# Performance work log

Hardware: AMD Instinct MI355X
Metric: run time of the kernel (lower is better)

## Reference

```python
import jax, jax.numpy as jnp
import numpy as np

N_NODES = 100_000
N_EDGES = 1_600_000
N_GRAPHS = 512
D_NODE = 128
H = 128
L_EXTRA = 2  # model_layer - 1


def _bn(x, g, b, eps=1e-5):
    # BatchNorm1d, training-mode math (biased batch variance), eval dropout = identity
    mu = jnp.mean(x, axis=0)
    var = jnp.var(x, axis=0)
    return g * (x - mu) * jax.lax.rsqrt(var + eps) + b


def _gin_conv(x, src, dst, W1, b1, bng, bnb, W2, b2):
    # GINConv (eps=0): mlp(x + sum_{j->i} x_j); mlp = Lin -> BN -> ReLU -> Lin
    agg = jax.ops.segment_sum(x[src], dst, num_segments=x.shape[0])
    h = x + agg
    h = jax.nn.relu(_bn(h @ W1 + b1, bng, bnb))
    return h @ W2 + b2


def setup_inputs():
    key = jax.random.key(0)
    ks = jax.random.split(key, 24)
    s = 0.05
    d = {}
    d["x"] = jax.random.normal(ks[0], (N_NODES, D_NODE), dtype=jnp.float32)
    d["edge_index"] = jax.random.randint(ks[1], (2, N_EDGES), 0, N_NODES, dtype=jnp.int32)
    d["batch"] = jnp.sort(jax.random.randint(ks[2], (N_NODES,), 0, N_GRAPHS, dtype=jnp.int32))
    d["vn_emb"] = jax.random.normal(ks[3], (1, H)) * s
    # conv1 MLP: Linear(D_NODE, 2H) -> BN -> ReLU -> Linear(2H, H)
    d["c1_W1"] = jax.random.normal(ks[4], (D_NODE, 2 * H)) * s
    d["c1_b1"] = jnp.zeros((2 * H,))
    d["c1_bng"] = jnp.ones((2 * H,))
    d["c1_bnb"] = jnp.zeros((2 * H,))
    d["c1_W2"] = jax.random.normal(ks[5], (2 * H, H)) * s
    d["c1_b2"] = jnp.zeros((H,))
    d["bn1_g"] = jnp.ones((H,))
    d["bn1_b"] = jnp.zeros((H,))
    # stacked extra GIN layers (model_layer - 1)
    d["cW1"] = jax.random.normal(ks[6], (L_EXTRA, H, 2 * H)) * s
    d["cb1"] = jnp.zeros((L_EXTRA, 2 * H))
    d["cbng"] = jnp.ones((L_EXTRA, 2 * H))
    d["cbnb"] = jnp.zeros((L_EXTRA, 2 * H))
    d["cW2"] = jax.random.normal(ks[7], (L_EXTRA, 2 * H, H)) * s
    d["cb2"] = jnp.zeros((L_EXTRA, H))
    d["bns_g"] = jnp.ones((L_EXTRA, H))
    d["bns_b"] = jnp.zeros((L_EXTRA, H))
    # virtual node MLP: Lin(H,2H)->BN->ReLU->Lin(2H,H)->BN->ReLU->Dropout
    d["vW1"] = jax.random.normal(ks[8], (H, 2 * H)) * s
    d["vb1"] = jnp.zeros((2 * H,))
    d["vbn1_g"] = jnp.ones((2 * H,))
    d["vbn1_b"] = jnp.zeros((2 * H,))
    d["vW2"] = jax.random.normal(ks[9], (2 * H, H)) * s
    d["vb2"] = jnp.zeros((H,))
    d["vbn2_g"] = jnp.ones((H,))
    d["vbn2_b"] = jnp.zeros((H,))
    return d


def reference(x, edge_index, batch, vn_emb, c1_W1, c1_b1, c1_bng, c1_bnb, c1_W2, c1_b2,
              bn1_g, bn1_b, cW1, cb1, cbng, cbnb, cW2, cb2, bns_g, bns_b,
              vW1, vb1, vbn1_g, vbn1_b, vW2, vb2, vbn2_g, vbn2_b):
    src, dst = edge_index[0], edge_index[1]
    # virtual node feature per graph: Embedding(1, H) indexed with zeros
    vfeat = jnp.broadcast_to(vn_emb[0], (N_GRAPHS, H))
    # layer 1: dropout is identity in eval mode
    post = jax.nn.relu(_bn(_gin_conv(x, src, dst, c1_W1, c1_b1, c1_bng, c1_bnb, c1_W2, c1_b2), bn1_g, bn1_b))
    for i in range(L_EXTRA):
        post = post + vfeat[batch]                       # virtual-node broadcast
        post = _bn(_gin_conv(post, src, dst, cW1[i], cb1[i], cbng[i], cbnb[i], cW2[i], cb2[i]), bns_g[i], bns_b[i])
        if i < L_EXTRA - 1:
            post = jax.nn.relu(post)
            pooled = jax.ops.segment_sum(post, batch, num_segments=N_GRAPHS)  # GlobalAddPool
            z = pooled + vfeat
            z = jax.nn.relu(_bn(z @ vW1 + vb1, vbn1_g, vbn1_b))
            vfeat = jax.nn.relu(_bn(z @ vW2 + vb2, vbn2_g, vbn2_b))
    # readout: global mean pool over nodes per graph
    counts = jax.ops.segment_sum(jnp.ones((x.shape[0],), post.dtype), batch, num_segments=N_GRAPHS)
    out = jax.ops.segment_sum(post, batch, num_segments=N_GRAPHS) / jnp.maximum(counts, 1.0)[:, None]
    return out
```

## Files before the change

### kernel.cpp

```cpp
#include <hip/hip_runtime.h>

#define NN 100000
#define NE 1600000
#define NG 512
#define DH 128
#define DH2 256
#define SCB 98
#define NSTRIPE 32

typedef __attribute__((ext_vector_type(8))) _Float16 h8;
typedef __attribute__((ext_vector_type(2))) _Float16 h2;
typedef __attribute__((ext_vector_type(4))) float f4;

static inline size_t align256(size_t x) { return (x + 255) & ~size_t(255); }

__global__ __launch_bounds__(256) void countslot_k(const int* __restrict__ ei,
                                                   int* __restrict__ cursor,
                                                   int* __restrict__ slot) {
    int i = blockIdx.x * blockDim.x + threadIdx.x;
    int stride = gridDim.x * blockDim.x;
    for (int e = i; e < NE; e += stride)
        slot[e] = atomicAdd(&cursor[ei[NE + e]], 1);
}

__global__ __launch_bounds__(256) void place_k(const int* __restrict__ ei,
                                               const int* __restrict__ rowptr,
                                               const int* __restrict__ slot,
                                               int* __restrict__ esrc) {
    int i = blockIdx.x * blockDim.x + threadIdx.x;
    int stride = gridDim.x * blockDim.x;
    for (int e = i; e < NE; e += stride)
        esrc[rowptr[ei[NE + e]] + slot[e]] = ei[e];
}

__global__ void gbound_k(const int* __restrict__ batch, int* __restrict__ gcnt) {
    int g = blockIdx.x * blockDim.x + threadIdx.x;
    if (g >= NG) return;
    int lo = 0, hi = NN;
    while (lo < hi) { int m = (lo + hi) >> 1; if (batch[m] < g) lo = m + 1; else hi = m; }
    int b0 = lo;
    lo = 0; hi = NN;
    int g1 = g + 1;
    while (lo < hi) { int m = (lo + hi) >> 1; if (batch[m] < g1) lo = m + 1; else hi = m; }
    gcnt[g] = lo - b0;
}

__global__ __launch_bounds__(256) void scan1_k(const int* __restrict__ deg,
                                               int* __restrict__ part) {
    int i0 = blockIdx.x * 1024 + threadIdx.x * 4;
    int s = 0;
    if (i0 < NN) {
        int4 v = *(const int4*)(deg + i0);
        s = v.x + v.y + v.z + v.w;
    }
#pragma unroll
    for (int o = 1; o < 64; o <<= 1) s += __shfl_xor(s, o);
    __shared__ int ws[4];
    if ((threadIdx.x & 63) == 0) ws[threadIdx.x >> 6] = s;
    __syncthreads();
    if (threadIdx.x == 0) part[blockIdx.x] = ws[0] + ws[1] + ws[2] + ws[3];
}

__global__ void scan2_k(int* __restrict__ part, int* __restrict__ rowptr) {
    int t = threadIdx.x;
    int v = (t < SCB) ? part[t] : 0;
    int s = v;
#pragma unroll
    for (int o = 1; o < 64; o <<= 1) {
        int u = __shfl_up(s, o);
        if ((t & 63) >= o) s += u;
    }
    __shared__ int wtot[2];
    if ((t & 63) == 63) wtot[t >> 6] = s;
    __syncthreads();
    if (t >= 64) s += wtot[0];
    if (t < SCB) part[t] = s - v;
    if (t == SCB - 1) rowptr[NN] = s;
}

__global__ __launch_bounds__(256) void scan3_k(const int* __restrict__ deg,
                                               const int* __restrict__ part,
                                               int* __restrict__ rowptr) {
    int t = threadIdx.x;
    int i0 = blockIdx.x * 1024 + t * 4;
    int4 v = {0, 0, 0, 0};
    if (i0 < NN) v = *(const int4*)(deg + i0);
    int s = v.x + v.y + v.z + v.w;
    __shared__ int sc[256];
    sc[t] = s;
    __syncthreads();
    for (int o = 1; o < 256; o <<= 1) {
        int add = (t >= o) ? sc[t - o] : 0;
        __syncthreads();
        sc[t] += add;
        __syncthreads();
    }
    int excl = (t ? sc[t - 1] : 0) + part[blockIdx.x];
    if (i0 < NN) {
        int4 r;
        r.x = excl;
        r.y = excl + v.x;
        r.z = excl + v.x + v.y;
        r.w = excl + v.x + v.y + v.z;
        *(int4*)(rowptr + i0) = r;
    }
}

__global__ void castx_k(const float* __restrict__ x, _Float16* __restrict__ xh) {
    int i = blockIdx.x * blockDim.x + threadIdx.x;
    if (i >= NN * 16) return;
    const float4* s = (const float4*)x + i * 2;
    float4 p = s[0], q = s[1];
    h8 h = {(_Float16)p.x, (_Float16)p.y, (_Float16)p.z, (_Float16)p.w,
            (_Float16)q.x, (_Float16)q.y, (_Float16)q.z, (_Float16)q.w};
    ((h8*)xh)[i] = h;
}

__global__ void vinit_k(const float* __restrict__ emb, _Float16* __restrict__ vfeat) {
    int i = blockIdx.x * blockDim.x + threadIdx.x;
    if (i < NG * DH) vfeat[i] = (_Float16)emb[i & (DH - 1)];
}

__global__ void zin_k(const float* __restrict__ pooled, const _Float16* __restrict__ vf,
                      _Float16* __restrict__ zb) {
    int i = blockIdx.x * blockDim.x + threadIdx.x;
    if (i < NG * DH) zb[i] = (_Float16)(pooled[i] + (float)vf[i]);
}

__global__ void addvn_k(_Float16* __restrict__ x, const _Float16* __restrict__ vfeat,
                        const int* __restrict__ batch) {
    int i = blockIdx.x * blockDim.x + threadIdx.x;
    if (i >= NN * 16) return;
    int row = i >> 4;
    int bg = batch[row];
    h8 u = ((h8*)x)[i];
    h8 v = ((const h8*)vfeat)[bg * 16 + (i & 15)];
    h8 o;
#pragma unroll
    for (int e = 0; e < 8; e++) o[e] = (_Float16)((float)u[e] + (float)v[e]);
    ((h8*)x)[i] = o;
}

__global__ void finalout_k(const float* __restrict__ pooled2, const int* __restrict__ gcnt,
                           float* __restrict__ outp) {
    int i = blockIdx.x * blockDim.x + threadIdx.x;
    if (i >= NG * DH) return;
    float cnt = (float)gcnt[i >> 7];
    outp[i] = pooled2[i] / fmaxf(cnt, 1.0f);
}

struct WPack {
    const float* w[8];
    _Float16* wt[8];
    int K[8];
    int N[8];
};
__global__ void wtrans_k(WPack p) {
    int id = blockIdx.z;
    const float* W = p.w[id];
    _Float16* Wt = p.wt[id];
    int K = p.K[id], N = p.N[id];
    int n0 = blockIdx.x * 32, k0 = blockIdx.y * 32;
    if (n0 >= N || k0 >= K) return;
    __shared__ float t[32][33];
    int tx = threadIdx.x & 31, ty = threadIdx.x >> 5;
    for (int i = 0; i < 32; i += 8)
        t[ty + i][tx] = W[(size_t)(k0 + ty + i) * N + n0 + tx];
    __syncthreads();
    for (int i = 0; i < 32; i += 8)
        Wt[(size_t)(n0 + ty + i) * K + k0 + tx] = (_Float16)t[tx][ty + i];
}

__global__ __launch_bounds__(256) void agg_k(const _Float16* __restrict__ xin,
                                             const int* __restrict__ rowptr,
                                             const int* __restrict__ esrc,
                                             _Float16* __restrict__ out) {
    int wave = threadIdx.x >> 6, lane = threadIdx.x & 63;
    int node = blockIdx.x * 4 + wave;
    if (node >= NN) return;
    const h2* xr = (const h2*)xin;
    h2 self = xr[(size_t)node * 64 + lane];
    float a0 = (float)self.x, a1 = (float)self.y;
    int beg = rowptr[node], end = rowptr[node + 1];
    int j = beg;
    for (; j + 7 < end; j += 8) {
        int s0 = esrc[j],     s1 = esrc[j + 1], s2 = esrc[j + 2], s3 = esrc[j + 3];
        int s4 = esrc[j + 4], s5 = esrc[j + 5], s6 = esrc[j + 6], s7 = esrc[j + 7];
        h2 u0 = xr[(size_t)s0 * 64 + lane];
        h2 u1 = xr[(size_t)s1 * 64 + lane];
        h2 u2 = xr[(size_t)s2 * 64 + lane];
        h2 u3 = xr[(size_t)s3 * 64 + lane];
        h2 u4 = xr[(size_t)s4 * 64 + lane];
        h2 u5 = xr[(size_t)s5 * 64 + lane];
        h2 u6 = xr[(size_t)s6 * 64 + lane];
        h2 u7 = xr[(size_t)s7 * 64 + lane];
        a0 += ((float)u0.x + (float)u1.x) + ((float)u2.x + (float)u3.x)
            + ((float)u4.x + (float)u5.x) + ((float)u6.x + (float)u7.x);
        a1 += ((float)u0.y + (float)u1.y) + ((float)u2.y + (float)u3.y)
            + ((float)u4.y + (float)u5.y) + ((float)u6.y + (float)u7.y);
    }
    for (; j < end; j++) {
        h2 u = xr[(size_t)esrc[j] * 64 + lane];
        a0 += (float)u.x; a1 += (float)u.y;
    }
    h2 o; o.x = (_Float16)a0; o.y = (_Float16)a1;
    ((h2*)out)[(size_t)node * 64 + lane] = o;
}

__global__ __launch_bounds__(256, 2) void gemmA_k(
        const _Float16* __restrict__ A, const _Float16* __restrict__ Wt,
        const float* __restrict__ bias, _Float16* __restrict__ C,
        float* __restrict__ csum, float* __restrict__ csq, int M) {
    constexpr int K = 128, NCF = 256;
    constexpr int LDA = K + 8;
    __shared__ __align__(16) _Float16 As[128 * LDA];
    __shared__ __align__(16) _Float16 Ws[128 * LDA];
    const int tid = threadIdx.x;
    const int lane = tid & 63;
    const int wave = tid >> 6;
    const int wr = wave & 1, wc = wave >> 1;
    const int lm = lane & 15, lq = lane >> 4;
    const int mB = blockIdx.x * 128;

    const int sr = tid >> 4;
    const int sc = (tid & 15) * 8;
#pragma unroll
    for (int rr = 0; rr < 128; rr += 16) {
        int gr = mB + rr + sr; if (gr >= M) gr = M - 1;
        *(h8*)&As[(rr + sr) * LDA + sc] = *(const h8*)&A[(size_t)gr * K + sc];
    }
#pragma unroll
    for (int rr = 0; rr < 128; rr += 16)
        *(h8*)&Ws[(rr + sr) * LDA + sc] = *(const h8*)&Wt[(size_t)(rr + sr) * K + sc];
    __syncthreads();

    f4 acc[4][8];
#pragma unroll
    for (int i = 0; i < 4; i++)
#pragma unroll
        for (int jj = 0; jj < 8; jj++) acc[i][jj] = (f4){0.f, 0.f, 0.f, 0.f};
#pragma unroll
    for (int ct = 0; ct < 2; ct++) {
        if (ct) {
            __syncthreads();
#pragma unroll
            for (int rr = 0; rr < 128; rr += 16)
                *(h8*)&Ws[(rr + sr) * LDA + sc] =
                    *(const h8*)&Wt[(size_t)(128 + rr + sr) * K + sc];
            __syncthreads();
        }
        const int n0w = wc * 64;
#pragma unroll
        for (int ks = 0; ks < 4; ks++) {
            h8 af[4], bf[4];
#pragma unroll
            for (int t = 0; t < 4; t++) {
                af[t] = *(const h8*)&As[(wr * 64 + t * 16 + lm) * LDA + ks * 32 + lq * 8];
                bf[t] = *(const h8*)&Ws[(n0w + t * 16 + lm) * LDA + ks * 32 + lq * 8];
            }
#pragma unroll
            for (int i = 0; i < 4; i++)
#pragma unroll
                for (int j = 0; j < 4; j++)
                    acc[i][ct * 4 + j] =
                        __builtin_amdgcn_mfma_f32_16x16x32_f16(af[i], bf[j], acc[i][ct * 4 + j], 0, 0, 0);
        }
    }

    float bv[8];
#pragma unroll
    for (int jj = 0; jj < 8; jj++) bv[jj] = bias[(jj >> 2) * 128 + wc * 64 + (jj & 3) * 16 + lm];
    float ls[8] = {0, 0, 0, 0, 0, 0, 0, 0}, lsq[8] = {0, 0, 0, 0, 0, 0, 0, 0};
    _Float16* Cs = As;
    const int trow = tid >> 4;
    const int tcol = (tid & 15) * 8;
#pragma unroll
    for (int half = 0; half < 2; half++) {
        __syncthreads();
#pragma unroll
        for (int i = 0; i < 4; i++) {
            int row = wr * 64 + i * 16 + lq * 4;
#pragma unroll
            for (int j = 0; j < 4; j++) {
                int jj = half * 4 + j;
#pragma unroll
                for (int r = 0; r < 4; r++) {
                    float v = acc[i][jj][r] + bv[jj];
                    Cs[(row + r) * LDA + wc * 64 + j * 16 + lm] = (_Float16)v;
                    if (mB + row + r < M) { ls[jj] += v; lsq[jj] += v * v; }
                }
            }
        }
        __syncthreads();
#pragma unroll
        for (int p = 0; p < 8; p++) {
            int row = p * 16 + trow;
            int grow = mB + row;
            if (grow < M) {
                h8 v = *(const h8*)&Cs[row * LDA + tcol];
                *(h8*)&C[(size_t)grow * NCF + half * 128 + tcol] = v;
            }
        }
    }
    const int stripe = blockIdx.x & (NSTRIPE - 1);
#pragma unroll
    for (int jj = 0; jj < 8; jj++) {
        float s = ls[jj], q = lsq[jj];
        s += __shfl_xor(s, 16); s += __shfl_xor(s, 32);
        q += __shfl_xor(q, 16); q += __shfl_xor(q, 32);
        if (lq == 0) {
            int col = (jj >> 2) * 128 + wc * 64 + (jj & 3) * 16 + lm;
            atomicAdd(&csum[stripe * NCF + col], s);
            atomicAdd(&csq[stripe * NCF + col], q);
        }
    }
}

__global__ __launch_bounds__(256, 2) void gemmB_k(
        const _Float16* __restrict__ A, const _Float16* __restrict__ Wt,
        const float* __restrict__ bias, _Float16* __restrict__ C,
        float* __restrict__ csum, float* __restrict__ csq, int M,
        const float* __restrict__ csumIn, const float* __restrict__ csqIn,
        const float* __restrict__ g, const float* __restrict__ b) {
    constexpr int K = 256, NCF = 128, BK = 128;
    constexpr int LDA = BK + 8;
    __shared__ __align__(16) _Float16 As[128 * LDA];
    __shared__ __align__(16) _Float16 Ws[128 * LDA];
    __shared__ float s_sc[256], s_sh[256];
    const int tid = threadIdx.x;
    const int lane = tid & 63;
    const int wave = tid >> 6;
    const int wr = wave & 1, wc = wave >> 1;
    const int lm = lane & 15, lq = lane >> 4;
    const int mB = blockIdx.x * 128;
    const int n0 = wc * 64;

    {
        float s = 0.f, q = 0.f;
        for (int st = 0; st < NSTRIPE; st++) {
            s += csumIn[st * 256 + tid];
            q += csqIn[st * 256 + tid];
        }
        float invM = 1.0f / (float)M;
        float mean = s * invM;
        float var = q * invM - mean * mean;
        float scv = g[tid] * rsqrtf(var + 1e-5f);
        s_sc[tid] = scv;
        s_sh[tid] = b[tid] - mean * scv;
    }
    __syncthreads();

    f4 acc[4][4];
#pragma unroll
    for (int i = 0; i < 4; i++)
#pragma unroll
        for (int j = 0; j < 4; j++) acc[i][j] = (f4){0.f, 0.f, 0.f, 0.f};

    const int sr = tid >> 4;
    const int sc = (tid & 15) * 8;

    for (int kc = 0; kc < K; kc += BK) {
        if (kc) __syncthreads();
        float bscv[8], bshv[8];
#pragma unroll
        for (int e = 0; e < 8; e++) {
            bscv[e] = s_sc[kc + sc + e];
            bshv[e] = s_sh[kc + sc + e];
        }
#pragma unroll
        for (int rr = 0; rr < 128; rr += 16) {
            int gr = mB + rr + sr; if (gr >= M) gr = M - 1;
            h8 h = *(const h8*)&A[(size_t)gr * K + kc + sc];
#pragma unroll
            for (int e = 0; e < 8; e++)
                h[e] = (_Float16)fmaxf((float)h[e] * bscv[e] + bshv[e], 0.f);
            *(h8*)&As[(rr + sr) * LDA + sc] = h;
        }
#pragma unroll
        for (int rr = 0; rr < 128; rr += 16)
            *(h8*)&Ws[(rr + sr) * LDA + sc] =
                *(const h8*)&Wt[(size_t)(rr + sr) * K + kc + sc];
        __syncthreads();
#pragma unroll
        for (int ks = 0; ks < BK / 32; ks++) {
            h8 af[4], bf[4];
#pragma unroll
            for (int t = 0; t < 4; t++) {
                af[t] = *(const h8*)&As[(wr * 64 + t * 16 + lm) * LDA + ks * 32 + lq * 8];
                bf[t] = *(const h8*)&Ws[(n0 + t * 16 + lm) * LDA + ks * 32 + lq * 8];
            }
#pragma unroll
            for (int i = 0; i < 4; i++)
#pragma unroll
                for (int j = 0; j < 4; j++)
                    acc[i][j] = __builtin_amdgcn_mfma_f32_16x16x32_f16(af[i], bf[j], acc[i][j], 0, 0, 0);
        }
    }

    float bv[4];
#pragma unroll
    for (int j = 0; j < 4; j++) bv[j] = bias[n0 + j * 16 + lm];
    float ls[4] = {0, 0, 0, 0}, lsq[4] = {0, 0, 0, 0};
    __syncthreads();
    _Float16* Cs = As;
#pragma unroll
    for (int i = 0; i < 4; i++) {
        int row = wr * 64 + i * 16 + lq * 4;
        bool rv[4];
#pragma unroll
        for (int r = 0; r < 4; r++) rv[r] = (mB + row + r) < M;
#pragma unroll
        for (int j = 0; j < 4; j++) {
#pragma unroll
            for (int r = 0; r < 4; r++) {
                float v = acc[i][j][r] + bv[j];
                Cs[(row + r) * LDA + wc * 64 + j * 16 + lm] = (_Float16)v;
                if (rv[r]) { ls[j] += v; lsq[j] += v * v; }
            }
        }
    }
    const int stripe = blockIdx.x & (NSTRIPE - 1);
#pragma unroll
    for (int j = 0; j < 4; j++) {
        float s = ls[j], q = lsq[j];
        s += __shfl_xor(s, 16); s += __shfl_xor(s, 32);
        q += __shfl_xor(q, 16); q += __shfl_xor(q, 32);
        if (lq == 0) {
            atomicAdd(&csum[stripe * NCF + n0 + j * 16 + lm], s);
            atomicAdd(&csq[stripe * NCF + n0 + j * 16 + lm], q);
        }
    }
    __syncthreads();
    const int trow = tid >> 4;
    const int tcol = (tid & 15) * 8;
#pragma unroll
    for (int p = 0; p < 8; p++) {
        int row = p * 16 + trow;
        int grow = mB + row;
        if (grow < M) {
            h8 v = *(const h8*)&Cs[row * LDA + tcol];
            *(h8*)&C[(size_t)grow * NCF + tcol] = v;
        }
    }
}

__global__ void bnrelu_k(const _Float16* __restrict__ in, _Float16* __restrict__ out,
                         const float* __restrict__ csum, const float* __restrict__ csq,
                         const float* __restrict__ g, const float* __restrict__ b,
                         const _Float16* __restrict__ vfeat, const int* __restrict__ batch,
                         int M) {
    constexpr int PER = 16;
    __shared__ float s_sc[128], s_sh[128];
    if (threadIdx.x < 128) {
        int col = threadIdx.x;
        float s = 0.f, q = 0.f;
        for (int st = 0; st < NSTRIPE; st++) {
            s += csum[st * 128 + col];
            q += csq[st * 128 + col];
        }
        float invM = 1.0f / (float)M;
        float mean = s * invM;
        float var = q * invM - mean * mean;
        float scv = g[col] * rsqrtf(var + 1e-5f);
        s_sc[col] = scv;
        s_sh[col] = b[col] - mean * scv;
    }
    __syncthreads();
    int tid = blockIdx.x * blockDim.x + threadIdx.x;
    int c8 = tid % PER;
    int c0 = c8 * 8;
    float sc[8], sh[8];
#pragma unroll
    for (int e = 0; e < 8; e++) { sc[e] = s_sc[c0 + e]; sh[e] = s_sh[c0 + e]; }
    int total = M * PER;
    int stride = gridDim.x * blockDim.x;
    for (int i = tid; i < total; i += stride) {
        int row = i / PER;
        h8 u = ((const h8*)in)[i];
        h8 w;
        bool vn = (vfeat != nullptr);
        if (vn) w = ((const h8*)vfeat)[batch[row] * PER + c8];
        h8 o;
#pragma unroll
        for (int e = 0; e < 8; e++) {
            float vv = fmaxf((float)u[e] * sc[e] + sh[e], 0.f);
            if (vn) vv += (float)w[e];
            o[e] = (_Float16)vv;
        }
        ((h8*)out)[i] = o;
    }
}

__global__ __launch_bounds__(256) void bnpool_k(
        const _Float16* __restrict__ in, _Float16* __restrict__ out,
        const float* __restrict__ csum, const float* __restrict__ csq,
        const float* __restrict__ g, const float* __restrict__ b,
        const int* __restrict__ batch, float* __restrict__ pooled,
        int M, int relu) {
    __shared__ float s_sc[128], s_sh[128];
    if (threadIdx.x < 128) {
        int col = threadIdx.x;
        float s = 0.f, q = 0.f;
        for (int st = 0; st < NSTRIPE; st++) {
            s += csum[st * 128 + col];
            q += csq[st * 128 + col];
        }
        float invM = 1.0f / (float)M;
        float mean = s * invM;
        float var = q * invM - mean * mean;
        float scv = g[col] * rsqrtf(var + 1e-5f);
        s_sc[col] = scv;
        s_sh[col] = b[col] - mean * scv;
    }
    __syncthreads();
    int t = threadIdx.x;
    int c0 = (t & 63) * 2;
    int r0 = blockIdx.x * 128 + (t >> 6) * 32;
    float sc0 = s_sc[c0], h0 = s_sh[c0];
    float sc1 = s_sc[c0 + 1], h1 = s_sh[c0 + 1];
    int rend = r0 + 32; if (rend > M) rend = M;
    float a0 = 0.f, a1 = 0.f; int cur = -1;
    int r = r0;
    for (; r + 1 < rend; r += 2) {
        h2 ua = ((const h2*)in)[(size_t)r * 64 + (c0 >> 1)];
        h2 ub = ((const h2*)in)[(size_t)(r + 1) * 64 + (c0 >> 1)];
        int bga = batch[r], bgb = batch[r + 1];
        float va0 = (float)ua.x * sc0 + h0, va1 = (float)ua.y * sc1 + h1;
        float vb0 = (float)ub.x * sc0 + h0, vb1 = (float)ub.y * sc1 + h1;
        if (relu) {
            va0 = fmaxf(va0, 0.f); va1 = fmaxf(va1, 0.f);
            vb0 = fmaxf(vb0, 0.f); vb1 = fmaxf(vb1, 0.f);
        }
        if (out) {
            h2 oa; oa.x = (_Float16)va0; oa.y = (_Float16)va1;
            h2 ob; ob.x = (_Float16)vb0; ob.y = (_Float16)vb1;
            ((h2*)out)[(size_t)r * 64 + (c0 >> 1)] = oa;
            ((h2*)out)[(size_t)(r + 1) * 64 + (c0 >> 1)] = ob;
        }
        if (bga != cur) {
            if (cur >= 0) {
                atomicAdd(&pooled[(size_t)cur * DH + c0], a0);
                atomicAdd(&pooled[(size_t)cur * DH + c0 + 1], a1);
            }
            cur = bga; a0 = 0.f; a1 = 0.f;
        }
        a0 += va0; a1 += va1;
        if (bgb != cur) {
            atomicAdd(&pooled[(size_t)cur * DH + c0], a0);
            atomicAdd(&pooled[(size_t)cur * DH + c0 + 1], a1);
            cur = bgb; a0 = 0.f; a1 = 0.f;
        }
        a0 += vb0; a1 += vb1;
    }
    for (; r < rend; r++) {
        h2 u = ((const h2*)in)[(size_t)r * 64 + (c0 >> 1)];
        float v0 = (float)u.x * sc0 + h0;
        float v1 = (float)u.y * sc1 + h1;
        if (relu) { v0 = fmaxf(v0, 0.f); v1 = fmaxf(v1, 0.f); }
        if (out) { h2 o; o.x = (_Float16)v0; o.y = (_Float16)v1; ((h2*)out)[(size_t)r * 64 + (c0 >> 1)] = o; }
        int bg = batch[r];
        if (bg != cur) {
            if (cur >= 0) {
                atomicAdd(&pooled[(size_t)cur * DH + c0], a0);
                atomicAdd(&pooled[(size_t)cur * DH + c0 + 1], a1);
            }
            cur = bg; a0 = 0.f; a1 = 0.f;
        }
        a0 += v0; a1 += v1;
    }
    if (cur >= 0) {
        atomicAdd(&pooled[(size_t)cur * DH + c0], a0);
        atomicAdd(&pooled[(size_t)cur * DH + c0 + 1], a1);
    }
}

extern "C" void kernel_launch(void* const* d_in, const int* in_sizes, int n_in,
                              void* d_out, int out_size, void* d_ws, size_t ws_size,
                              hipStream_t stream) {
    const float* x      = (const float*)d_in[0];
    const int*   ei     = (const int*)d_in[1];
    const int*   batch  = (const int*)d_in[2];
    const float* vn_emb = (const float*)d_in[3];
    const float* c1_W1  = (const float*)d_in[4];
    const float* c1_b1  = (const float*)d_in[5];
    const float* c1_bng = (const float*)d_in[6];
    const float* c1_bnb = (const float*)d_in[7];
    const float* c1_W2  = (const float*)d_in[8];
    const float* c1_b2  = (const float*)d_in[9];
    const float* bn1_g  = (const float*)d_in[10];
    const float* bn1_b  = (const float*)d_in[11];
    const float* cW1    = (const float*)d_in[12];
    const float* cb1    = (const float*)d_in[13];
    const float* cbng   = (const float*)d_in[14];
    const float* cbnb   = (const float*)d_in[15];
    const float* cW2    = (const float*)d_in[16];
    const float* cb2    = (const float*)d_in[17];
    const float* bns_g  = (const float*)d_in[18];
    const float* bns_b  = (const float*)d_in[19];
    const float* vW1    = (const float*)d_in[20];
    const float* vb1    = (const float*)d_in[21];
    const float* vbn1_g = (const float*)d_in[22];
    const float* vbn1_b = (const float*)d_in[23];
    const float* vW2    = (const float*)d_in[24];
    const float* vb2    = (const float*)d_in[25];
    const float* vbn2_g = (const float*)d_in[26];
    const float* vbn2_b = (const float*)d_in[27];
    float* outp = (float*)d_out;
    (void)in_sizes; (void)n_in; (void)out_size; (void)ws_size;

    char* w = (char*)d_ws;
    size_t off = 0;
    auto carve = [&](size_t bytes) -> void* {
        void* p = w + off; off = align256(off + bytes); return p;
    };
    int*   cursor  = (int*)carve((size_t)NN * 4);
    float* pooled  = (float*)carve((size_t)NG * DH * 4);
    float* pooled2 = (float*)carve((size_t)NG * DH * 4);
    float *sA[3], *qA[3], *sB[3], *qB[3], *sV1, *qV1, *sV2, *qV2;
    for (int i = 0; i < 3; i++) {
        sA[i] = (float*)carve((size_t)NSTRIPE * 256 * 4);
        qA[i] = (float*)carve((size_t)NSTRIPE * 256 * 4);
    }
    for (int i = 0; i < 3; i++) {
        sB[i] = (float*)carve((size_t)NSTRIPE * 128 * 4);
        qB[i] = (float*)carve((size_t)NSTRIPE * 128 * 4);
    }
    sV1 = (float*)carve((size_t)NSTRIPE * 256 * 4);
    qV1 = (float*)carve((size_t)NSTRIPE * 256 * 4);
    sV2 = (float*)carve((size_t)NSTRIPE * 128 * 4);
    qV2 = (float*)carve((size_t)NSTRIPE * 128 * 4);
    size_t zbytes = off;
    int*   gcnt    = (int*)carve((size_t)NG * 4);
    int*   rowptr  = (int*)carve((size_t)(NN + 1) * 4);
    int*   slot    = (int*)carve((size_t)NE * 4);
    int*   esrc    = (int*)carve((size_t)NE * 4);
    int*   part    = (int*)carve((size_t)SCB * 4);
    _Float16* vfeat = (_Float16*)carve((size_t)NG * DH * 2);
    _Float16* zin   = (_Float16*)carve((size_t)NG * DH * 2);
    _Float16* zb    = (_Float16*)carve((size_t)NG * DH2 * 2);
    _Float16* vraw  = (_Float16*)carve((size_t)NG * DH * 2);
    _Float16* xh    = (_Float16*)carve((size_t)NN * DH * 2);
    _Float16* hb    = (_Float16*)carve((size_t)NN * DH * 2);
    _Float16* b1    = (_Float16*)carve((size_t)NN * DH2 * 2);
    _Float16* abuf  = (_Float16*)carve((size_t)NN * DH * 2);
    _Float16* Wt[8];
    for (int i = 0; i < 8; i++) Wt[i] = (_Float16*)carve((size_t)DH * DH2 * 2);

    WPack wp;
    wp.w[0] = c1_W1;            wp.K[0] = 128; wp.N[0] = 256;
    wp.w[1] = c1_W2;            wp.K[1] = 256; wp.N[1] = 128;
    wp.w[2] = cW1;              wp.K[2] = 128; wp.N[2] = 256;
    wp.w[3] = cW2;              wp.K[3] = 256; wp.N[3] = 128;
    wp.w[4] = cW1 + 128 * 256;  wp.K[4] = 128; wp.N[4] = 256;
    wp.w[5] = cW2 + 256 * 128;  wp.K[5] = 256; wp.N[5] = 128;
    wp.w[6] = vW1;              wp.K[6] = 128; wp.N[6] = 256;
    wp.w[7] = vW2;              wp.K[7] = 256; wp.N[7] = 128;
    for (int i = 0; i < 8; i++) wp.wt[i] = Wt[i];

    const int GB = (NN + 127) / 128;

    hipMemsetAsync(d_ws, 0, zbytes, stream);
    countslot_k<<<782, 256, 0, stream>>>(ei, cursor, slot);
    scan1_k<<<SCB, 256, 0, stream>>>(cursor, part);
    scan2_k<<<1, 128, 0, stream>>>(part, rowptr);
    scan3_k<<<SCB, 256, 0, stream>>>(cursor, part, rowptr);
    place_k<<<782, 256, 0, stream>>>(ei, rowptr, slot, esrc);
    gbound_k<<<2, 256, 0, stream>>>(batch, gcnt);
    wtrans_k<<<dim3(8, 8, 8), 256, 0, stream>>>(wp);
    vinit_k<<<(NG * DH + 255) / 256, 256, 0, stream>>>(vn_emb, vfeat);
    castx_k<<<(NN * 16 + 255) / 256, 256, 0, stream>>>(x, xh);

    agg_k<<<NN / 4, 256, 0, stream>>>(xh, rowptr, esrc, hb);
    gemmA_k<<<GB, 256, 0, stream>>>(hb, Wt[0], c1_b1, b1, sA[0], qA[0], NN);
    gemmB_k<<<GB, 256, 0, stream>>>(b1, Wt[1], c1_b2, abuf, sB[0], qB[0], NN,
                                    sA[0], qA[0], c1_bng, c1_bnb);
    bnrelu_k<<<2048, 256, 0, stream>>>(abuf, abuf, sB[0], qB[0], bn1_g, bn1_b,
                                       vfeat, batch, NN);

    agg_k<<<NN / 4, 256, 0, stream>>>(abuf, rowptr, esrc, hb);
    gemmA_k<<<GB, 256, 0, stream>>>(hb, Wt[2], cb1, b1, sA[1], qA[1], NN);
    gemmB_k<<<GB, 256, 0, stream>>>(b1, Wt[3], cb2, abuf, sB[1], qB[1], NN,
                                    sA[1], qA[1], cbng, cbnb);
    bnpool_k<<<GB, 256, 0, stream>>>(abuf, abuf, sB[1], qB[1], bns_g, bns_b,
                                     batch, pooled, NN, 1);

    zin_k<<<(NG * DH + 255) / 256, 256, 0, stream>>>(pooled, vfeat, zin);
    gemmA_k<<<4, 256, 0, stream>>>(zin, Wt[6], vb1, zb, sV1, qV1, NG);
    gemmB_k<<<4, 256, 0, stream>>>(zb, Wt[7], vb2, vraw, sV2, qV2, NG,
                                   sV1, qV1, vbn1_g, vbn1_b);
    bnrelu_k<<<32, 256, 0, stream>>>(vraw, vfeat, sV2, qV2, vbn2_g, vbn2_b,
                                     nullptr, nullptr, NG);

    addvn_k<<<(NN * 16 + 255) / 256, 256, 0, stream>>>(abuf, vfeat, batch);
    agg_k<<<NN / 4, 256, 0, stream>>>(abuf, rowptr, esrc, hb);
    gemmA_k<<<GB, 256, 0, stream>>>(hb, Wt[4], cb1 + 256, b1, sA[2], qA[2], NN);
    gemmB_k<<<GB, 256, 0, stream>>>(b1, Wt[5], cb2 + 128, abuf, sB[2], qB[2], NN,
                                    sA[2], qA[2], cbng + 256, cbnb + 256);
    bnpool_k<<<GB, 256, 0, stream>>>(abuf, nullptr, sB[2], qB[2],
                                     bns_g + 128, bns_b + 128, batch, pooled2, NN, 0);

    finalout_k<<<(NG * DH + 255) / 256, 256, 0, stream>>>(pooled2, gcnt, outp);
}
```

Before: 719.9 us.

## Halve GEMM row tiles to 64 and raise occupancy; merge small setup kernels

Both GEMM kernels now process 64-row tiles instead of 128, with a 2x2 wave layout. This halves the accumulators and the A shared-memory tile, and launch bounds are raised to allow 3 blocks per CU. The goal is better occupancy and better load balance across the 256 CUs, since about 1563 blocks now launch instead of about 782. In exchange, each block re-reads the full weight tile for half as many rows, which doubles total weight traffic. Separately, the graph-boundary search is folded into scan2 and the virtual-node init into castx, which removes two kernel launches.

After: 703.8 us. 1.02x faster.

```diff
diff --git a/kernel.cpp b/kernel.cpp
--- a/kernel.cpp
+++ b/kernel.cpp
@@ -33,18 +33,6 @@
         esrc[rowptr[ei[NE + e]] + slot[e]] = ei[e];
 }
 
-__global__ void gbound_k(const int* __restrict__ batch, int* __restrict__ gcnt) {
-    int g = blockIdx.x * blockDim.x + threadIdx.x;
-    if (g >= NG) return;
-    int lo = 0, hi = NN;
-    while (lo < hi) { int m = (lo + hi) >> 1; if (batch[m] < g) lo = m + 1; else hi = m; }
-    int b0 = lo;
-    lo = 0; hi = NN;
-    int g1 = g + 1;
-    while (lo < hi) { int m = (lo + hi) >> 1; if (batch[m] < g1) lo = m + 1; else hi = m; }
-    gcnt[g] = lo - b0;
-}
-
 __global__ __launch_bounds__(256) void scan1_k(const int* __restrict__ deg,
                                                int* __restrict__ part) {
     int i0 = blockIdx.x * 1024 + threadIdx.x * 4;
@@ -61,21 +49,36 @@
     if (threadIdx.x == 0) part[blockIdx.x] = ws[0] + ws[1] + ws[2] + ws[3];
 }
 
-__global__ void scan2_k(int* __restrict__ part, int* __restrict__ rowptr) {
+__global__ void scan2_k(int* __restrict__ part, int* __restrict__ rowptr,
+                        const int* __restrict__ batch, int* __restrict__ gcnt) {
     int t = threadIdx.x;
-    int v = (t < SCB) ? part[t] : 0;
-    int s = v;
-#pragma unroll
-    for (int o = 1; o < 64; o <<= 1) {
-        int u = __shfl_up(s, o);
-        if ((t & 63) >= o) s += u;
-    }
     __shared__ int wtot[2];
-    if ((t & 63) == 63) wtot[t >> 6] = s;
-    __syncthreads();
-    if (t >= 64) s += wtot[0];
-    if (t < SCB) part[t] = s - v;
-    if (t == SCB - 1) rowptr[NN] = s;
+    int v = 0, s = 0;
+    if (t < 128) {
+        v = (t < SCB) ? part[t] : 0;
+        s = v;
+#pragma unroll
+        for (int o = 1; o < 64; o <<= 1) {
+            int u = __shfl_up(s, o);
+            if ((t & 63) >= o) s += u;
+        }
+        if ((t & 63) == 63) wtot[t >> 6] = s;
+    }
+    __syncthreads();
+    if (t < 128) {
+        if (t >= 64) s += wtot[0];
+        if (t < SCB) part[t] = s - v;
+        if (t == SCB - 1) rowptr[NN] = s;
+    }
+    for (int g = t; g < NG; g += 256) {
+        int lo = 0, hi = NN;
+        while (lo < hi) { int m = (lo + hi) >> 1; if (batch[m] < g) lo = m + 1; else hi = m; }
+        int b0 = lo;
+        lo = 0; hi = NN;
+        int g1 = g + 1;
+        while (lo < hi) { int m = (lo + hi) >> 1; if (batch[m] < g1) lo = m + 1; else hi = m; }
+        gcnt[g] = lo - b0;
+    }
 }
 
 __global__ __launch_bounds__(256) void scan3_k(const int* __restrict__ deg,
@@ -106,19 +109,21 @@
     }
 }
 
-__global__ void castx_k(const float* __restrict__ x, _Float16* __restrict__ xh) {
+__global__ void castx_k(const float* __restrict__ x, _Float16* __restrict__ xh,
+                        const float* __restrict__ emb, _Float16* __restrict__ vfeat) {
     int i = blockIdx.x * blockDim.x + threadIdx.x;
+    if (i < NG * 16) {
+        const float* e = emb + (i & 15) * 8;
+        h8 v = {(_Float16)e[0], (_Float16)e[1], (_Float16)e[2], (_Float16)e[3],
+                (_Float16)e[4], (_Float16)e[5], (_Float16)e[6], (_Float16)e[7]};
+        ((h8*)vfeat)[i] = v;
+    }
     if (i >= NN * 16) return;
     const float4* s = (const float4*)x + i * 2;
     float4 p = s[0], q = s[1];
     h8 h = {(_Float16)p.x, (_Float16)p.y, (_Float16)p.z, (_Float16)p.w,
             (_Float16)q.x, (_Float16)q.y, (_Float16)q.z, (_Float16)q.w};
     ((h8*)xh)[i] = h;
-}
-
-__global__ void vinit_k(const float* __restrict__ emb, _Float16* __restrict__ vfeat) {
-    int i = blockIdx.x * blockDim.x + threadIdx.x;
-    if (i < NG * DH) vfeat[i] = (_Float16)emb[i & (DH - 1)];
 }
 
 __global__ void zin_k(const float* __restrict__ pooled, const _Float16* __restrict__ vf,
@@ -207,25 +212,26 @@
     ((h2*)out)[(size_t)node * 64 + lane] = o;
 }
 
-__global__ __launch_bounds__(256, 2) void gemmA_k(
+__global__ __launch_bounds__(256, 3) void gemmA_k(
         const _Float16* __restrict__ A, const _Float16* __restrict__ Wt,
         const float* __restrict__ bias, _Float16* __restrict__ C,
         float* __restrict__ csum, float* __restrict__ csq, int M) {
     constexpr int K = 128, NCF = 256;
     constexpr int LDA = K + 8;
-    __shared__ __align__(16) _Float16 As[128 * LDA];
+    __shared__ __align__(16) _Float16 As[64 * LDA];
     __shared__ __align__(16) _Float16 Ws[128 * LDA];
     const int tid = threadIdx.x;
     const int lane = tid & 63;
     const int wave = tid >> 6;
-    const int wr = wave & 1, wc = wave >> 1;
+    const int wr = wave >> 1;
+    const int wc = wave & 1;
     const int lm = lane & 15, lq = lane >> 4;
-    const int mB = blockIdx.x * 128;
+    const int mB = blockIdx.x * 64;
 
     const int sr = tid >> 4;
     const int sc = (tid & 15) * 8;
 #pragma unroll
-    for (int rr = 0; rr < 128; rr += 16) {
+    for (int rr = 0; rr < 64; rr += 16) {
         int gr = mB + rr + sr; if (gr >= M) gr = M - 1;
         *(h8*)&As[(rr + sr) * LDA + sc] = *(const h8*)&A[(size_t)gr * K + sc];
     }
@@ -234,9 +240,9 @@
         *(h8*)&Ws[(rr + sr) * LDA + sc] = *(const h8*)&Wt[(size_t)(rr + sr) * K + sc];
     __syncthreads();
 
-    f4 acc[4][8];
-#pragma unroll
-    for (int i = 0; i < 4; i++)
+    f4 acc[2][8];
+#pragma unroll
+    for (int i = 0; i < 2; i++)
 #pragma unroll
         for (int jj = 0; jj < 8; jj++) acc[i][jj] = (f4){0.f, 0.f, 0.f, 0.f};
 #pragma unroll
@@ -249,17 +255,17 @@
                     *(const h8*)&Wt[(size_t)(128 + rr + sr) * K + sc];
             __syncthreads();
         }
-        const int n0w = wc * 64;
 #pragma unroll
         for (int ks = 0; ks < 4; ks++) {
-            h8 af[4], bf[4];
-#pragma unroll
-            for (int t = 0; t < 4; t++) {
-                af[t] = *(const h8*)&As[(wr * 64 + t * 16 + lm) * LDA + ks * 32 + lq * 8];
-                bf[t] = *(const h8*)&Ws[(n0w + t * 16 + lm) * LDA + ks * 32 + lq * 8];
-            }
-#pragma unroll
-            for (int i = 0; i < 4; i++)
+            h8 af[2], bf[4];
+#pragma unroll
+            for (int i = 0; i < 2; i++)
+                af[i] = *(const h8*)&As[(wr * 32 + i * 16 + lm) * LDA + ks * 32 + lq * 8];
+#pragma unroll
+            for (int j = 0; j < 4; j++)
+                bf[j] = *(const h8*)&Ws[(wc * 64 + j * 16 + lm) * LDA + ks * 32 + lq * 8];
+#pragma unroll
+            for (int i = 0; i < 2; i++)
 #pragma unroll
                 for (int j = 0; j < 4; j++)
                     acc[i][ct * 4 + j] =
@@ -278,8 +284,8 @@
     for (int half = 0; half < 2; half++) {
         __syncthreads();
 #pragma unroll
-        for (int i = 0; i < 4; i++) {
-            int row = wr * 64 + i * 16 + lq * 4;
+        for (int i = 0; i < 2; i++) {
+            int row = wr * 32 + i * 16 + lq * 4;
 #pragma unroll
             for (int j = 0; j < 4; j++) {
                 int jj = half * 4 + j;
@@ -293,7 +299,7 @@
         }
         __syncthreads();
 #pragma unroll
-        for (int p = 0; p < 8; p++) {
+        for (int p = 0; p < 4; p++) {
             int row = p * 16 + trow;
             int grow = mB + row;
             if (grow < M) {
@@ -316,7 +322,7 @@
     }
 }
 
-__global__ __launch_bounds__(256, 2) void gemmB_k(
+__global__ __launch_bounds__(256, 3) void gemmB_k(
         const _Float16* __restrict__ A, const _Float16* __restrict__ Wt,
         const float* __restrict__ bias, _Float16* __restrict__ C,
         float* __restrict__ csum, float* __restrict__ csq, int M,
@@ -324,15 +330,17 @@
         const float* __restrict__ g, const float* __restrict__ b) {
     constexpr int K = 256, NCF = 128, BK = 128;
     constexpr int LDA = BK + 8;
-    __shared__ __align__(16) _Float16 As[128 * LDA];
-    __shared__ __align__(16) _Float16 Ws[128 * LDA];
+    constexpr int LDW = BK + 4;
+    __shared__ __align__(16) _Float16 As[64 * LDA];
+    __shared__ __align__(16) _Float16 Ws[128 * LDW];
     __shared__ float s_sc[256], s_sh[256];
     const int tid = threadIdx.x;
     const int lane = tid & 63;
     const int wave = tid >> 6;
-    const int wr = wave & 1, wc = wave >> 1;
+    const int wr = wave >> 1;
+    const int wc = wave & 1;
     const int lm = lane & 15, lq = lane >> 4;
-    const int mB = blockIdx.x * 128;
+    const int mB = blockIdx.x * 64;
     const int n0 = wc * 64;
 
     {
@@ -350,9 +358,9 @@
     }
     __syncthreads();
 
-    f4 acc[4][4];
-#pragma unroll
-    for (int i = 0; i < 4; i++)
+    f4 acc[2][4];
+#pragma unroll
+    for (int i = 0; i < 2; i++)
 #pragma unroll
         for (int j = 0; j < 4; j++) acc[i][j] = (f4){0.f, 0.f, 0.f, 0.f};
 
@@ -368,7 +376,7 @@
             bshv[e] = s_sh[kc + sc + e];
         }
 #pragma unroll
-        for (int rr = 0; rr < 128; rr += 16) {
+        for (int rr = 0; rr < 64; rr += 16) {
             int gr = mB + rr + sr; if (gr >= M) gr = M - 1;
             h8 h = *(const h8*)&A[(size_t)gr * K + kc + sc];
 #pragma unroll
@@ -378,19 +386,20 @@
         }
 #pragma unroll
         for (int rr = 0; rr < 128; rr += 16)
-            *(h8*)&Ws[(rr + sr) * LDA + sc] =
+            *(h8*)&Ws[(rr + sr) * LDW + sc] =
                 *(const h8*)&Wt[(size_t)(rr + sr) * K + kc + sc];
         __syncthreads();
 #pragma unroll
         for (int ks = 0; ks < BK / 32; ks++) {
-            h8 af[4], bf[4];
-#pragma unroll
-            for (int t = 0; t < 4; t++) {
-                af[t] = *(const h8*)&As[(wr * 64 + t * 16 + lm) * LDA + ks * 32 + lq * 8];
-                bf[t] = *(const h8*)&Ws[(n0 + t * 16 + lm) * LDA + ks * 32 + lq * 8];
-            }
-#pragma unroll
-            for (int i = 0; i < 4; i++)
+            h8 af[2], bf[4];
+#pragma unroll
+            for (int i = 0; i < 2; i++)
+                af[i] = *(const h8*)&As[(wr * 32 + i * 16 + lm) * LDA + ks * 32 + lq * 8];
+#pragma unroll
+            for (int j = 0; j < 4; j++)
+                bf[j] = *(const h8*)&Ws[(n0 + j * 16 + lm) * LDW + ks * 32 + lq * 8];
+#pragma unroll
+            for (int i = 0; i < 2; i++)
 #pragma unroll
                 for (int j = 0; j < 4; j++)
                     acc[i][j] = __builtin_amdgcn_mfma_f32_16x16x32_f16(af[i], bf[j], acc[i][j], 0, 0, 0);
@@ -404,8 +413,8 @@
     __syncthreads();
     _Float16* Cs = As;
 #pragma unroll
-    for (int i = 0; i < 4; i++) {
-        int row = wr * 64 + i * 16 + lq * 4;
+    for (int i = 0; i < 2; i++) {
+        int row = wr * 32 + i * 16 + lq * 4;
         bool rv[4];
 #pragma unroll
         for (int r = 0; r < 4; r++) rv[r] = (mB + row + r) < M;
@@ -434,7 +443,7 @@
     const int trow = tid >> 4;
     const int tcol = (tid & 15) * 8;
 #pragma unroll
-    for (int p = 0; p < 8; p++) {
+    for (int p = 0; p < 4; p++) {
         int row = p * 16 + trow;
         int grow = mB + row;
         if (grow < M) {
@@ -657,45 +666,45 @@
     wp.w[7] = vW2;              wp.K[7] = 256; wp.N[7] = 128;
     for (int i = 0; i < 8; i++) wp.wt[i] = Wt[i];
 
-    const int GB = (NN + 127) / 128;
+    const int GB64 = (NN + 63) / 64;
+    const int GB   = (NN + 127) / 128;
+    const int GV64 = (NG + 63) / 64;
 
     hipMemsetAsync(d_ws, 0, zbytes, stream);
     countslot_k<<<782, 256, 0, stream>>>(ei, cursor, slot);
     scan1_k<<<SCB, 256, 0, stream>>>(cursor, part);
-    scan2_k<<<1, 128, 0, stream>>>(part, rowptr);
+    scan2_k<<<1, 256, 0, stream>>>(part, rowptr, batch, gcnt);
     scan3_k<<<SCB, 256, 0, stream>>>(cursor, part, rowptr);
     place_k<<<782, 256, 0, stream>>>(ei, rowptr, slot, esrc);
-    gbound_k<<<2, 256, 0, stream>>>(batch, gcnt);
     wtrans_k<<<dim3(8, 8, 8), 256, 0, stream>>>(wp);
-    vinit_k<<<(NG * DH + 255) / 256, 256, 0, stream>>>(vn_emb, vfeat);
-    castx_k<<<(NN * 16 + 255) / 256, 256, 0, stream>>>(x, xh);
+    castx_k<<<(NN * 16 + 255) / 256, 256, 0, stream>>>(x, xh, vn_emb, vfeat);
 
     agg_k<<<NN / 4, 256, 0, stream>>>(xh, rowptr, esrc, hb);
-    gemmA_k<<<GB, 256, 0, stream>>>(hb, Wt[0], c1_b1, b1, sA[0], qA[0], NN);
-    gemmB_k<<<GB, 256, 0, stream>>>(b1, Wt[1], c1_b2, abuf, sB[0], qB[0], NN,
-                                    sA[0], qA[0], c1_bng, c1_bnb);
+    gemmA_k<<<GB64, 256, 0, stream>>>(hb, Wt[0], c1_b1, b1, sA[0], qA[0], NN);
+    gemmB_k<<<GB64, 256, 0, stream>>>(b1, Wt[1], c1_b2, abuf, sB[0], qB[0], NN,
+                                      sA[0], qA[0], c1_bng, c1_bnb);
     bnrelu_k<<<2048, 256, 0, stream>>>(abuf, abuf, sB[0], qB[0], bn1_g, bn1_b,
                                        vfeat, batch, NN);
 
     agg_k<<<NN / 4, 256, 0, stream>>>(abuf, rowptr, esrc, hb);
-    gemmA_k<<<GB, 256, 0, stream>>>(hb, Wt[2], cb1, b1, sA[1], qA[1], NN);
-    gemmB_k<<<GB, 256, 0, stream>>>(b1, Wt[3], cb2, abuf, sB[1], qB[1], NN,
-                                    sA[1], qA[1], cbng, cbnb);
+    gemmA_k<<<GB64, 256, 0, stream>>>(hb, Wt[2], cb1, b1, sA[1], qA[1], NN);
+    gemmB_k<<<GB64, 256, 0, stream>>>(b1, Wt[3], cb2, abuf, sB[1], qB[1], NN,
+                                      sA[1], qA[1], cbng, cbnb);
     bnpool_k<<<GB, 256, 0, stream>>>(abuf, abuf, sB[1], qB[1], bns_g, bns_b,
                                      batch, pooled, NN, 1);
 
     zin_k<<<(NG * DH + 255) / 256, 256, 0, stream>>>(pooled, vfeat, zin);
-    gemmA_k<<<4, 256, 0, stream>>>(zin, Wt[6], vb1, zb, sV1, qV1, NG);
-    gemmB_k<<<4, 256, 0, stream>>>(zb, Wt[7], vb2, vraw, sV2, qV2, NG,
-                                   sV1, qV1, vbn1_g, vbn1_b);
+    gemmA_k<<<GV64, 256, 0, stream>>>(zin, Wt[6], vb1, zb, sV1, qV1, NG);
+    gemmB_k<<<GV64, 256, 0, stream>>>(zb, Wt[7], vb2, vraw, sV2, qV2, NG,
+                                      sV1, qV1, vbn1_g, vbn1_b);
     bnrelu_k<<<32, 256, 0, stream>>>(vraw, vfeat, sV2, qV2, vbn2_g, vbn2_b,
                                      nullptr, nullptr, NG);
 
     addvn_k<<<(NN * 16 + 255) / 256, 256, 0, stream>>>(abuf, vfeat, batch);
     agg_k<<<NN / 4, 256, 0, stream>>>(abuf, rowptr, esrc, hb);
-    gemmA_k<<<GB, 256, 0, stream>>>(hb, Wt[4], cb1 + 256, b1, sA[2], qA[2], NN);
-    gemmB_k<<<GB, 256, 0, stream>>>(b1, Wt[5], cb2 + 128, abuf, sB[2], qB[2], NN,
-                                    sA[2], qA[2], cbng + 256, cbnb + 256);
+    gemmA_k<<<GB64, 256, 0, stream>>>(hb, Wt[4], cb1 + 256, b1, sA[2], qA[2], NN);
+    gemmB_k<<<GB64, 256, 0, stream>>>(b1, Wt[5], cb2 + 128, abuf, sB[2], qB[2], NN,
+                                      sA[2], qA[2], cbng + 256, cbnb + 256);
     bnpool_k<<<GB, 256, 0, stream>>>(abuf, nullptr, sB[2], qB[2],
                                      bns_g + 128, bns_b + 128, batch, pooled2, NN, 0);
 
```
